# Kernel tuning notes

Hardware: AMD Instinct MI355X
Metric: run time of the kernel (lower is better)

The kernel has to match this reference:

```python
import jax, jax.numpy as jnp
import numpy as np

V, E, H, D, DFF, NB, C, B, T = 32000, 512, 256, 512, 2048, 4, 16, 32, 512
PAD, BOS, EOS = 0, 1, 2


def positional_encoding(t, d):
    pos = jnp.arange(t, dtype=jnp.float32)[:, None]
    i = jnp.arange(0, d, 2, dtype=jnp.float32)
    div = jnp.exp(-(jnp.log(10000.0)) * i / d)
    pe = jnp.zeros((t, d), jnp.float32)
    pe = pe.at[:, 0::2].set(jnp.sin(pos * div))
    pe = pe.at[:, 1::2].set(jnp.cos(pos * div))
    return pe


def layernorm(x, g, b, eps=1e-5):
    mu = jnp.mean(x, -1, keepdims=True)
    var = jnp.mean((x - mu) ** 2, -1, keepdims=True)
    return (x - mu) * jax.lax.rsqrt(var + eps) * g + b


def gru_dir(xs, w_ih, w_hh, b_ih, b_hh, reverse):
    # xs: (B,T,E); precompute input projections for all t (one big GEMM)
    gi = jnp.einsum('bte,ge->btg', xs, w_ih) + b_ih  # (B,T,3H)
    h0 = jnp.zeros((xs.shape[0], H), xs.dtype)

    def step(h, gi_t):
        gh = h @ w_hh.T + b_hh
        i_r, i_z, i_n = jnp.split(gi_t, 3, -1)
        h_r, h_z, h_n = jnp.split(gh, 3, -1)
        r = jax.nn.sigmoid(i_r + h_r)
        z = jax.nn.sigmoid(i_z + h_z)
        n = jnp.tanh(i_n + r * h_n)
        h_new = (1.0 - z) * n + z * h
        return h_new, h_new

    _, hs = jax.lax.scan(step, h0, jnp.swapaxes(gi, 0, 1), reverse=reverse)
    return jnp.swapaxes(hs, 0, 1)  # (B,T,H)


def forward(x, y, embed_W, w_ih_f, w_hh_f, b_ih_f, b_hh_f, w_ih_b, w_hh_b, b_ih_b, b_hh_b,
            ff_w1, ff_b1, ff_w2, ff_b2, ln_g, ln_b, fc_w, fc_b, trans):
    h = embed_W[x]                                   # (B,T,E)
    h = h + positional_encoding(h.shape[1], E)[None]
    hf = gru_dir(h, w_ih_f, w_hh_f, b_ih_f, b_hh_f, False)
    hb = gru_dir(h, w_ih_b, w_hh_b, b_ih_b, b_hh_b, True)
    h = jnp.concatenate([hf, hb], -1)                # (B,T,D)
    for i in range(NB):                              # FeedForward blocks (residual + LN)
        ff = jax.nn.relu(h @ ff_w1[i] + ff_b1[i]) @ ff_w2[i] + ff_b2[i]
        h = layernorm(h + ff, ln_g[i], ln_b[i])
    logits = h @ fc_w + fc_b                         # (B,T,C) emissions

    # --- CRF viterbi decode ---
    mask = (y != PAD)                                # (B,T) bool
    emit = jnp.swapaxes(logits, 0, 1)                # (T,B,C)
    m = jnp.swapaxes(mask, 0, 1)                     # (T,B)
    score0 = trans[BOS][None] + emit[0]              # (B,C)

    def vstep(score, inp):
        e_t, m_t = inp                               # (B,C), (B,)
        cand = score[:, :, None] + trans[None] + e_t[:, None, :]  # (B,prev,cur)
        new = jnp.max(cand, axis=1)
        bp = jnp.argmax(cand, axis=1)                # (B,C)
        new = jnp.where(m_t[:, None], new, score)
        return new, bp

    final, bps = jax.lax.scan(vstep, score0, (emit[1:], m[1:]))  # bps: (T-1,B,C)
    final = final + trans[:, EOS][None]
    best_score = jnp.max(final, -1)                  # (B,)
    last_tag = jnp.argmax(final, -1)                 # (B,)

    def back(tag, inp):
        bp_t, m_t = inp
        prev = jnp.take_along_axis(bp_t, tag[:, None], axis=1)[:, 0]
        prev = jnp.where(m_t, prev, tag)
        return prev, tag

    first_tag, rest = jax.lax.scan(back, last_tag, (bps, m[1:]), reverse=True)
    path = jnp.swapaxes(jnp.concatenate([first_tag[None], rest], 0), 0, 1)  # (B,T)
    return best_score, path


def setup_inputs():
    key = jax.random.key(0)
    ks = jax.random.split(key, 16)
    nrm = lambda k, sh, sc: jax.random.normal(k, sh, jnp.float32) * sc
    s = 1.0 / float(np.sqrt(H))
    inp = {}
    inp['x'] = jax.random.randint(ks[0], (B, T), 1, V)
    inp['y'] = jax.random.randint(ks[1], (B, T), 0, 13) + 3  # in [3,16): no pad/bos/eos
    inp['embed_W'] = nrm(ks[2], (V, E), 0.02)
    inp['w_ih_f'] = nrm(ks[3], (3 * H, E), s); inp['w_hh_f'] = nrm(ks[4], (3 * H, H), s)
    inp['b_ih_f'] = nrm(ks[5], (3 * H,), s); inp['b_hh_f'] = nrm(ks[6], (3 * H,), s)
    inp['w_ih_b'] = nrm(ks[7], (3 * H, E), s); inp['w_hh_b'] = nrm(ks[8], (3 * H, H), s)
    inp['b_ih_b'] = nrm(ks[9], (3 * H,), s); inp['b_hh_b'] = nrm(ks[10], (3 * H,), s)
    inp['ff_w1'] = nrm(ks[11], (NB, D, DFF), 1.0 / float(np.sqrt(D)))
    inp['ff_b1'] = jnp.zeros((NB, DFF), jnp.float32)
    inp['ff_w2'] = nrm(ks[12], (NB, DFF, D), 1.0 / float(np.sqrt(DFF)))
    inp['ff_b2'] = jnp.zeros((NB, D), jnp.float32)
    inp['ln_g'] = jnp.ones((NB, D), jnp.float32); inp['ln_b'] = jnp.zeros((NB, D), jnp.float32)
    inp['fc_w'] = nrm(ks[13], (D, C), 1.0 / float(np.sqrt(D)))
    inp['fc_b'] = jnp.zeros((C,), jnp.float32)
    inp['trans'] = nrm(ks[14], (C, C), 0.1)
    return inp


def reference(x, y, embed_W, w_ih_f, w_hh_f, b_ih_f, b_hh_f, w_ih_b, w_hh_b, b_ih_b, b_hh_b,
              ff_w1, ff_b1, ff_w2, ff_b2, ln_g, ln_b, fc_w, fc_b, trans):
    return forward(x, y, embed_W, w_ih_f, w_hh_f, b_ih_f, b_hh_f, w_ih_b, w_hh_b, b_ih_b, b_hh_b,
                   ff_w1, ff_b1, ff_w2, ff_b2, ln_g, ln_b, fc_w, fc_b, trans)
```

## Files before the change

### kernel.cpp

```cpp
#include <hip/hip_runtime.h>

#define DEV __device__ __forceinline__

using short8 = __attribute__((ext_vector_type(8))) short;
using f32x4  = __attribute__((ext_vector_type(4))) float;
using i32x4  = __attribute__((ext_vector_type(4))) int;

DEV float b2f(short s) {
  union { unsigned u; float f; } c;
  c.u = ((unsigned)(unsigned short)s) << 16;
  return c.f;
}
DEV short f2b(float f) {
  union { float f; unsigned u; } c; c.f = f;
  unsigned u = c.u + 0x7fffu + ((c.u >> 16) & 1u);
  return (short)(u >> 16);
}
DEV float fast_sigmoid(float x) {
  return __builtin_amdgcn_rcpf(1.f + __expf(-x));
}
DEV float fast_tanh(float x) {
  return 1.f - 2.f * __builtin_amdgcn_rcpf(1.f + __expf(2.f * x));
}
DEV void async_ld16(const void* g, void* lds) {
  __builtin_amdgcn_global_load_lds(
      (const __attribute__((address_space(1))) void*)(unsigned long long)g,
      (__attribute__((address_space(3))) void*)(unsigned)(unsigned long long)lds,
      16, 0, 0);
}

__global__ __launch_bounds__(256) void k_cvt2(const float* __restrict__ a, const float* __restrict__ b,
                                              short* __restrict__ oa, short* __restrict__ ob) {
  int blk = blockIdx.x;
  const float* in; short* out; int base;
  if (blk < 384) { in = a; out = oa; base = blk; }
  else           { in = b; out = ob; base = blk - 384; }
  int i = base * 256 + threadIdx.x;
  f32x4 v = *(const f32x4*)(in + (size_t)i * 4);
  short4 o;
#pragma unroll
  for (int j = 0; j < 4; j++) ((short*)&o)[j] = f2b(v[j]);
  *(short4*)(out + (size_t)i * 4) = o;
}

__global__ __launch_bounds__(256) void k_wq8(const float* __restrict__ wf,
                                             const float* __restrict__ wb,
                                             int* __restrict__ out) {
  int flat = blockIdx.x * 256 + threadIdx.x;
  int lane = flat & 63;
  int c = (flat >> 6) & 3;
  int t = flat >> 8;
  int g = t % 3;
  int t2 = t / 3;
  int v = t2 & 15, d = t2 >> 4;
  const float* w = d ? wb : wf;
  int row = g * 256 + v * 16 + (lane & 15);
  int k0 = c * 64 + (lane >> 4) * 16;
  const float* p = w + (size_t)row * 256 + k0;
  int pk[4];
#pragma unroll
  for (int i = 0; i < 4; i++) {
    f32x4 f = *(const f32x4*)(p + i * 4);
    int b0 = (int)__builtin_rintf(f[0] * 256.f);
    int b1 = (int)__builtin_rintf(f[1] * 256.f);
    int b2 = (int)__builtin_rintf(f[2] * 256.f);
    int b3 = (int)__builtin_rintf(f[3] * 256.f);
    b0 = min(127, max(-127, b0)); b1 = min(127, max(-127, b1));
    b2 = min(127, max(-127, b2)); b3 = min(127, max(-127, b3));
    pk[i] = (b0 & 255) | ((b1 & 255) << 8) | ((b2 & 255) << 16) | ((b3 & 255) << 24);
  }
  *(int4*)(out + (size_t)flat * 4) = *(int4*)pk;
}

__global__ __launch_bounds__(256) void k_embed(const int* __restrict__ x,
                                               const float* __restrict__ W,
                                               short* __restrict__ h0) {
  int flat = blockIdx.x * 256 + threadIdx.x;
  int row  = flat >> 6;
  int e0   = (flat & 63) << 3;
  int tok  = x[row];
  int t    = row & 511;
  const float* wp = W + (size_t)tok * 512 + e0;
  float v[8];
  *(f32x4*)v       = *(const f32x4*)(wp);
  *(f32x4*)(v + 4) = *(const f32x4*)(wp + 4);
  short8 o;
#pragma unroll
  for (int i = 0; i < 8; i += 2) {
    float f = expf(-9.210340371976184f * (float)(e0 + i) * (1.f / 512.f));
    float ang = (float)t * f;
    o[i]     = f2b(v[i]     + sinf(ang));
    o[i + 1] = f2b(v[i + 1] + cosf(ang));
  }
  *(short8*)(h0 + (size_t)flat * 8) = o;
}

template <int MODE>
__global__ __launch_bounds__(256) void k_gemm(const short* __restrict__ A,
    const short* __restrict__ B, const float* __restrict__ bias,
    const float* __restrict__ bias2,
    float* __restrict__ Cf, short* __restrict__ Cb, int M, int N, int K) {
  __shared__ short smA[8192];
  __shared__ short smB[8192];
  const int tid = threadIdx.x, lane = tid & 63, wave = tid >> 6;
  const int m15 = lane & 15, q8 = (lane >> 4) << 3;
  const int tn = N >> 7;
  const int bm = blockIdx.x / tn, bn = blockIdx.x % tn;
  const int wm = wave & 1, wn = wave >> 1;
  const f32x4 z4 = {0.f, 0.f, 0.f, 0.f};
  f32x4 acc[4][4];
#pragma unroll
  for (int i = 0; i < 4; i++)
#pragma unroll
    for (int j = 0; j < 4; j++) acc[i][j] = z4;

  for (int k0 = 0; k0 < K; k0 += 64) {
#pragma unroll
    for (int is = 0; is < 4; is++) {
      int c = is * 4 + wave;
      int mb = c & 7, kb = c >> 3;
      async_ld16(A + (size_t)(bm * 128 + mb * 16 + m15) * K + k0 + kb * 32 + q8, smA + c * 512);
      async_ld16(B + (size_t)(bn * 128 + mb * 16 + m15) * K + k0 + kb * 32 + q8, smB + c * 512);
    }
    __syncthreads();
#pragma unroll
    for (int kk = 0; kk < 2; kk++) {
      short8 af[4], bf[4];
#pragma unroll
      for (int i = 0; i < 4; i++)
        af[i] = *(const short8*)(smA + (kk * 8 + wm * 4 + i) * 512 + lane * 8);
#pragma unroll
      for (int j = 0; j < 4; j++)
        bf[j] = *(const short8*)(smB + (kk * 8 + wn * 4 + j) * 512 + lane * 8);
#pragma unroll
      for (int i = 0; i < 4; i++)
#pragma unroll
        for (int j = 0; j < 4; j++)
          acc[i][j] = __builtin_amdgcn_mfma_f32_16x16x32_bf16(af[i], bf[j], acc[i][j], 0, 0, 0);
    }
    __syncthreads();
  }
#pragma unroll
  for (int j = 0; j < 4; j++) {
    int col = bn * 128 + wn * 64 + j * 16 + m15;
    float bv;
    if (MODE == 3) bv = (col < 768) ? bias[col] : bias2[col - 768];
    else           bv = bias[col];
#pragma unroll
    for (int i = 0; i < 4; i++) {
      int row0 = bm * 128 + wm * 64 + i * 16 + ((lane >> 4) << 2);
#pragma unroll
      for (int r = 0; r < 4; r++) {
        float v = acc[i][j][r] + bv;
        int rr = row0 + r;
        if (MODE == 0) {
          Cf[(size_t)rr * N + col] = v;
        } else if (MODE == 1) {
          if (v < 0.f) v = 0.f;
          Cb[(size_t)rr * N + col] = f2b(v);
        } else {
          Cb[((size_t)((rr & 511) * 32 + (rr >> 9))) * 1536 + col] = f2b(v);
        }
      }
    }
  }
}

__global__ __launch_bounds__(1024) void k_gru(
    const int* __restrict__ wq8,
    const float* __restrict__ bhh_f, const float* __restrict__ bhh_b,
    const short* __restrict__ gi16,
    short* __restrict__ hcat16,
    const float* __restrict__ ff_w1, const float* __restrict__ ff_w2,
    short* __restrict__ w1t, short* __restrict__ w2t) {
  __shared__ __align__(16) char smem[16896];
  const int blk = blockIdx.x;
  const int tid = threadIdx.x;

  if (blk >= 16) {
    int sub = tid >> 8, stid = tid & 255;
    int tileid = (blk - 16) * 4 + sub;
    const float* in; short* out; int C, R, tm;
    if (tileid < 4096) { int mat = tileid >> 10; in = ff_w1 + (size_t)mat * 1048576;
                         out = w1t + (size_t)mat * 1048576; R = 512; C = 2048; tm = tileid & 1023; }
    else               { int mat = (tileid - 4096) >> 10; in = ff_w2 + (size_t)mat * 1048576;
                         out = w2t + (size_t)mat * 1048576; R = 2048; C = 512; tm = tileid & 1023; }
    float (*tile)[33] = (float(*)[33])(smem + sub * 4224);
    int ct = C >> 5;
    int bc = tm % ct, br = tm / ct;
    int r0 = br << 5, c0 = bc << 5;
    for (int i = stid; i < 1024; i += 256) {
      int r = i >> 5, c = i & 31;
      tile[r][c] = in[(size_t)(r0 + r) * C + c0 + c];
    }
    __syncthreads();
    for (int i = stid; i < 1024; i += 256) {
      int c = i >> 5, r = i & 31;
      out[(size_t)(c0 + c) * R + r0 + r] = f2b(tile[r][c]);
    }
    return;
  }

  char (*hb)[4096] = (char(*)[4096])smem;
  const int d = blk & 1, bg = blk >> 1;
  const int lane = tid & 63, v = tid >> 6;
  const int m15 = lane & 15, quad = lane >> 4;
  const int col = v * 16 + m15;
  const int brow = quad;
  const float* bhh = d ? bhh_b : bhh_f;
  const float SCL = 1.f / (127.f * 256.f);

  i32x4 Bq[3][4];
  {
    const i32x4* wp = (const i32x4*)wq8 + (size_t)(d * 16 + v) * (3 * 4 * 64);
#pragma unroll
    for (int g = 0; g < 3; g++)
#pragma unroll
      for (int c = 0; c < 4; c++)
        Bq[g][c] = wp[(g * 4 + c) * 64 + lane];
  }
  float bh[3];
#pragma unroll
  for (int g = 0; g < 3; g++) bh[g] = bhh[g * 256 + col];

  const int sw = (m15 & 7) << 4;
  const int aof0 = m15 * 256 + ((quad * 16 +   0) ^ sw);
  const int aof1 = m15 * 256 + ((quad * 16 +  64) ^ sw);
  const int aof2 = m15 * 256 + ((quad * 16 + 128) ^ sw);
  const int aof3 = m15 * 256 + ((quad * 16 + 192) ^ sw);
  const int wofs = brow * 256 + (col ^ (brow << 4));
  const int idx4 = m15 << 2;

  for (int i = tid; i < 2048; i += 1024) ((int*)hb)[i] = 0;

  const int t0 = d ? 511 : 0;
  const long gdelta = (long)(d ? -1 : 1) * 32 * 1536;
  const long hdelta = (long)(d ? -1 : 1) * 32 * 512;
  const short* gp = gi16 + ((size_t)t0 * 32 + bg * 4 + brow) * 1536 + d * 768 + col;
  short* hflush = hcat16 + ((size_t)t0 * 32 + bg * 4 + brow) * 512 + d * 256 + col;

  float gic0 = b2f(gp[0]), gic1 = b2f(gp[256]), gic2 = b2f(gp[512]);
  gp += gdelta;
  float hprev = 0.f;
  unsigned obuf[4] = {0u, 0u, 0u, 0u};
  const i32x4 zi = {0, 0, 0, 0};
  __syncthreads();

  for (int s = 0; s < 512; s++) {
    if ((s & 7) == 0 && s) {
      short* p = hflush;
#pragma unroll
      for (int k = 0; k < 8; k++) {
        *p = (short)(obuf[k >> 1] >> ((k & 1) * 16));
        p += hdelta;
      }
      hflush += 8 * hdelta;
    }
    short n0 = 0, n1 = 0, n2 = 0;
    if (s < 511) {
      n0 = gp[0]; n1 = gp[256]; n2 = gp[512];
      gp += gdelta;
    }
    const char* hs = hb[s & 1];
    i32x4 Af0 = *(const i32x4*)(hs + aof0);
    i32x4 Af1 = *(const i32x4*)(hs + aof1);
    i32x4 Af2 = *(const i32x4*)(hs + aof2);
    i32x4 Af3 = *(const i32x4*)(hs + aof3);
    i32x4 acc0 = zi, acc1 = zi, acc2 = zi;
    acc0 = __builtin_amdgcn_mfma_i32_16x16x64_i8(Af0, Bq[0][0], acc0, 0, 0, 0);
    acc1 = __builtin_amdgcn_mfma_i32_16x16x64_i8(Af0, Bq[1][0], acc1, 0, 0, 0);
    acc2 = __builtin_amdgcn_mfma_i32_16x16x64_i8(Af0, Bq[2][0], acc2, 0, 0, 0);
    acc0 = __builtin_amdgcn_mfma_i32_16x16x64_i8(Af1, Bq[0][1], acc0, 0, 0, 0);
    acc1 = __builtin_amdgcn_mfma_i32_16x16x64_i8(Af1, Bq[1][1], acc1, 0, 0, 0);
    acc2 = __builtin_amdgcn_mfma_i32_16x16x64_i8(Af1, Bq[2][1], acc2, 0, 0, 0);
    acc0 = __builtin_amdgcn_mfma_i32_16x16x64_i8(Af2, Bq[0][2], acc0, 0, 0, 0);
    acc1 = __builtin_amdgcn_mfma_i32_16x16x64_i8(Af2, Bq[1][2], acc1, 0, 0, 0);
    acc2 = __builtin_amdgcn_mfma_i32_16x16x64_i8(Af2, Bq[2][2], acc2, 0, 0, 0);
    acc0 = __builtin_amdgcn_mfma_i32_16x16x64_i8(Af3, Bq[0][3], acc0, 0, 0, 0);
    acc1 = __builtin_amdgcn_mfma_i32_16x16x64_i8(Af3, Bq[1][3], acc1, 0, 0, 0);
    acc2 = __builtin_amdgcn_mfma_i32_16x16x64_i8(Af3, Bq[2][3], acc2, 0, 0, 0);
    int r0 = __builtin_amdgcn_ds_bpermute(idx4, acc0[0]);
    int r1 = __builtin_amdgcn_ds_bpermute(idx4, acc0[1]);
    int r2 = __builtin_amdgcn_ds_bpermute(idx4, acc0[2]);
    int r3 = __builtin_amdgcn_ds_bpermute(idx4, acc0[3]);
    int z0 = __builtin_amdgcn_ds_bpermute(idx4, acc1[0]);
    int z1 = __builtin_amdgcn_ds_bpermute(idx4, acc1[1]);
    int z2 = __builtin_amdgcn_ds_bpermute(idx4, acc1[2]);
    int z3 = __builtin_amdgcn_ds_bpermute(idx4, acc1[3]);
    int n0i = __builtin_amdgcn_ds_bpermute(idx4, acc2[0]);
    int n1i = __builtin_amdgcn_ds_bpermute(idx4, acc2[1]);
    int n2i = __builtin_amdgcn_ds_bpermute(idx4, acc2[2]);
    int n3i = __builtin_amdgcn_ds_bpermute(idx4, acc2[3]);
    int igr = (quad & 2) ? ((quad & 1) ? r3 : r2) : ((quad & 1) ? r1 : r0);
    int igz = (quad & 2) ? ((quad & 1) ? z3 : z2) : ((quad & 1) ? z1 : z0);
    int ign = (quad & 2) ? ((quad & 1) ? n3i : n2i) : ((quad & 1) ? n1i : n0i);
    float r = fast_sigmoid(fmaf((float)igr, SCL, gic0 + bh[0]));
    float z = fast_sigmoid(fmaf((float)igz, SCL, gic1 + bh[1]));
    float n = fast_tanh(fmaf(r, fmaf((float)ign, SCL, bh[2]), gic2));
    float h = (1.f - z) * n + z * hprev;
    hprev = h;
    int hq = (int)__builtin_rintf(h * 127.f);
    hb[(s + 1) & 1][wofs] = (char)hq;
    unsigned hb16 = (unsigned)(unsigned short)f2b(h);
    int idx = s & 7;
    if ((idx & 1) == 0) obuf[idx >> 1] = hb16;
    else                obuf[idx >> 1] |= hb16 << 16;
    gic0 = b2f(n0); gic1 = b2f(n1); gic2 = b2f(n2);
    __syncthreads();
  }
  {
    short* p = hflush;
#pragma unroll
    for (int k = 0; k < 8; k++) {
      *p = (short)(obuf[k >> 1] >> ((k & 1) * 16));
      p += hdelta;
    }
  }
}

template <int FIRST>
__global__ __launch_bounds__(256) void k_ln(const float* __restrict__ hinf,
    const float* __restrict__ ff, const float* __restrict__ gw,
    const float* __restrict__ bw, float* __restrict__ hout, short* __restrict__ h16) {
  int row = blockIdx.x * 4 + (threadIdx.x >> 6);
  int lane = threadIdx.x & 63;
  size_t base = (size_t)row * 512 + lane * 8;
  f32x4 x0, x1;
  if (FIRST) {
    short8 hv = *(const short8*)(h16 + base);
#pragma unroll
    for (int i = 0; i < 4; i++) { x0[i] = b2f(hv[i]); x1[i] = b2f(hv[4 + i]); }
  } else {
    x0 = *(const f32x4*)(hinf + base);
    x1 = *(const f32x4*)(hinf + base + 4);
  }
  f32x4 y0 = *(const f32x4*)(ff + base);
  f32x4 y1 = *(const f32x4*)(ff + base + 4);
  x0 += y0; x1 += y1;
  float s = x0[0] + x0[1] + x0[2] + x0[3] + x1[0] + x1[1] + x1[2] + x1[3];
#pragma unroll
  for (int off = 32; off >= 1; off >>= 1) s += __shfl_xor(s, off);
  float mu = s * (1.f / 512.f);
  float vv = 0.f;
#pragma unroll
  for (int i = 0; i < 4; i++) { float d0 = x0[i] - mu, d1 = x1[i] - mu; vv += d0 * d0 + d1 * d1; }
#pragma unroll
  for (int off = 32; off >= 1; off >>= 1) vv += __shfl_xor(vv, off);
  float rs = rsqrtf(vv * (1.f / 512.f) + 1e-5f);
  int e = lane * 8;
  f32x4 g0 = *(const f32x4*)(gw + e), g1 = *(const f32x4*)(gw + e + 4);
  f32x4 bb0 = *(const f32x4*)(bw + e), bb1 = *(const f32x4*)(bw + e + 4);
  f32x4 o0, o1; short8 ob;
#pragma unroll
  for (int i = 0; i < 4; i++) {
    float a = (x0[i] - mu) * rs * g0[i] + bb0[i];
    float b = (x1[i] - mu) * rs * g1[i] + bb1[i];
    o0[i] = a; o1[i] = b; ob[i] = f2b(a); ob[4 + i] = f2b(b);
  }
  *(f32x4*)(hout + base) = o0;
  *(f32x4*)(hout + base + 4) = o1;
  *(short8*)(h16 + base) = ob;
}

__global__ __launch_bounds__(256) void k_fc(const float* __restrict__ h,
    const float* __restrict__ fcw, const float* __restrict__ bias,
    float* __restrict__ logits) {
  int row = blockIdx.x * 4 + (threadIdx.x >> 6);
  int lane = threadIdx.x & 63;
  int c = lane & 15, part = lane >> 4;
  const float* ph = h + (size_t)row * 512 + part * 128;
  const float* pw = fcw + (size_t)part * 128 * 16 + c;
  float acc = 0.f;
#pragma unroll 8
  for (int k = 0; k < 128; k += 4) {
    f32x4 hv = *(const f32x4*)(ph + k);
    acc += hv[0] * pw[(k) * 16] + hv[1] * pw[(k + 1) * 16]
         + hv[2] * pw[(k + 2) * 16] + hv[3] * pw[(k + 3) * 16];
  }
  acc += __shfl_xor(acc, 16);
  acc += __shfl_xor(acc, 32);
  if (part == 0) logits[(size_t)row * 16 + c] = acc + bias[c];
}

__global__ __launch_bounds__(64) void k_crf(const float* __restrict__ logits,
    const int* __restrict__ y, const float* __restrict__ trans,
    float* __restrict__ out) {
  __shared__ unsigned char bp[511][16];
  int b = blockIdx.x, lane = threadIdx.x;
  int cur = lane & 15, g = lane >> 4;
  float trr0 = trans[(4 * g + 0) * 16 + cur];
  float trr1 = trans[(4 * g + 1) * 16 + cur];
  float trr2 = trans[(4 * g + 2) * 16 + cur];
  float trr3 = trans[(4 * g + 3) * 16 + cur];
  const float* lg = logits + (size_t)b * 16;
  const int* yb = y + b * 512;
  float score = trans[16 + cur] + lg[cur];
  float e_next = lg[512 + cur];
  int y_next = yb[1];
  for (int t = 1; t < 512; t++) {
    float e = e_next; int ym = y_next;
    if (t < 511) { e_next = lg[(t + 1) * 512 + cur]; y_next = yb[t + 1]; }
    float s0 = __shfl(score, 4 * g + 0);
    float s1 = __shfl(score, 4 * g + 1);
    float s2 = __shfl(score, 4 * g + 2);
    float s3 = __shfl(score, 4 * g + 3);
    float best = s0 + trr0; int arg = 4 * g;
    float c1 = s1 + trr1; if (c1 > best) { best = c1; arg = 4 * g + 1; }
    float c2 = s2 + trr2; if (c2 > best) { best = c2; arg = 4 * g + 2; }
    float c3 = s3 + trr3; if (c3 > best) { best = c3; arg = 4 * g + 3; }
    float pv = __shfl_xor(best, 16); int pa = __shfl_xor(arg, 16);
    bool take = (lane & 16) ? (pv >= best) : (pv > best);
    if (take) { best = pv; arg = pa; }
    pv = __shfl_xor(best, 32); pa = __shfl_xor(arg, 32);
    take = (lane & 32) ? (pv >= best) : (pv > best);
    if (take) { best = pv; arg = pa; }
    if (lane < 16) bp[t - 1][cur] = (unsigned char)arg;
    float ns = best + e;
    if (ym == 0) ns = score;
    score = ns;
  }
  score += trans[cur * 16 + 2];
  float best = -3.4e38f; int argb = 0;
#pragma unroll
  for (int p = 0; p < 16; p++) {
    float sp = __shfl(score, p);
    if (sp > best) { best = sp; argb = p; }
  }
  __syncthreads();
  if (lane == 0) {
    out[b] = best;
    float* po = out + 32 + (size_t)b * 512;
    int tag = argb;
    po[511] = (float)tag;
    for (int t = 511; t >= 1; t--) {
      int prev = bp[t - 1][tag];
      if (yb[t] == 0) prev = tag;
      po[t - 1] = (float)prev;
      tag = prev;
    }
  }
}

extern "C" void kernel_launch(void* const* d_in, const int* in_sizes, int n_in,
                              void* d_out, int out_size, void* d_ws, size_t ws_size,
                              hipStream_t stream) {
  const int*   x      = (const int*)d_in[0];
  const int*   y      = (const int*)d_in[1];
  const float* embedW = (const float*)d_in[2];
  const float* w_ih_f = (const float*)d_in[3];
  const float* w_hh_f = (const float*)d_in[4];
  const float* b_ih_f = (const float*)d_in[5];
  const float* b_hh_f = (const float*)d_in[6];
  const float* w_ih_b = (const float*)d_in[7];
  const float* w_hh_b = (const float*)d_in[8];
  const float* b_ih_b = (const float*)d_in[9];
  const float* b_hh_b = (const float*)d_in[10];
  const float* ff_w1  = (const float*)d_in[11];
  const float* ff_b1  = (const float*)d_in[12];
  const float* ff_w2  = (const float*)d_in[13];
  const float* ff_b2  = (const float*)d_in[14];
  const float* ln_g   = (const float*)d_in[15];
  const float* ln_b   = (const float*)d_in[16];
  const float* fc_w   = (const float*)d_in[17];
  const float* fc_b   = (const float*)d_in[18];
  const float* trans  = (const float*)d_in[19];
  float* out = (float*)d_out;

  char* ws = (char*)d_ws;
  short* h0     = (short*)(ws + 0);
  short* gi16   = (short*)(ws + 16777216);
  short* mid    = (short*)(ws + 16777216);
  float* ffout  = (float*)(ws + 83886080);
  short* wihf16 = (short*)(ws + 117440512);
  short* wihb16 = (short*)(ws + 118226944);
  int*   wq8    = (int*)  (ws + 119013376);
  short* w1t    = (short*)(ws + 119799808);
  short* w2t    = (short*)(ws + 128188416);
  short* hcat16 = (short*)(ws + 136577024);
  float* hres   = (float*)(ws + 153354240);
  float* logits = (float*)(ws + 186908672);

  k_embed<<<4096, 256, 0, stream>>>(x, embedW, h0);
  k_cvt2<<<768, 256, 0, stream>>>(w_ih_f, w_ih_b, wihf16, wihb16);
  k_wq8<<<96, 256, 0, stream>>>(w_hh_f, w_hh_b, wq8);

  k_gemm<3><<<1536, 256, 0, stream>>>(h0, wihf16, b_ih_f, b_ih_b, nullptr, gi16, 16384, 1536, 512);

  k_gru<<<2064, 1024, 0, stream>>>(wq8, b_hh_f, b_hh_b, gi16, hcat16,
                                   ff_w1, ff_w2, w1t, w2t);

  for (int i = 0; i < 4; i++) {
    k_gemm<1><<<2048, 256, 0, stream>>>(hcat16, w1t + (size_t)i * 1048576, ff_b1 + i * 2048,
                                        nullptr, nullptr, mid, 16384, 2048, 512);
    k_gemm<0><<<512, 256, 0, stream>>>(mid, w2t + (size_t)i * 1048576, ff_b2 + i * 512,
                                       nullptr, ffout, nullptr, 16384, 512, 2048);
    if (i == 0)
      k_ln<1><<<4096, 256, 0, stream>>>(nullptr, ffout, ln_g, ln_b, hres, hcat16);
    else
      k_ln<0><<<4096, 256, 0, stream>>>(hres, ffout, ln_g + i * 512, ln_b + i * 512, hres, hcat16);
  }
  k_fc<<<4096, 256, 0, stream>>>(hres, fc_w, fc_b, logits);
  k_crf<<<32, 64, 0, stream>>>(logits, y, trans, out);
}
```

Before: 1.520 ms.

## Move FF weight transpose into input GEMM, vectorize epilogue, bf16 FF output

The FF weight transpose/convert work moves out of the GRU launch and into extra blocks of the input-projection GEMM, so the GRU kernel launches only its 16 recurrent blocks. The GEMM gains an XCD-aware block index remap, swaps MFMA operands so each lane owns four contiguous columns, and stores with vectorized short4/f32x4 writes. The second FF GEMM now writes bf16 instead of fp32, halving the traffic into layernorm at the cost of reduced precision in the residual add. The transpose no longer overlaps the serial GRU, which risks adding time on the critical path.

New measurement: 1.602 ms. 5.4% more time.

```diff
diff --git a/kernel.cpp b/kernel.cpp
--- a/kernel.cpp
+++ b/kernel.cpp
@@ -99,13 +99,43 @@
 __global__ __launch_bounds__(256) void k_gemm(const short* __restrict__ A,
     const short* __restrict__ B, const float* __restrict__ bias,
     const float* __restrict__ bias2,
-    float* __restrict__ Cf, short* __restrict__ Cb, int M, int N, int K) {
-  __shared__ short smA[8192];
-  __shared__ short smB[8192];
+    float* __restrict__ Cf, short* __restrict__ Cb, int M, int N, int K,
+    const float* __restrict__ tw1, const float* __restrict__ tw2,
+    short* __restrict__ w1t, short* __restrict__ w2t) {
+  __shared__ __align__(16) char smem[32768];
+  short* smA = (short*)smem;
+  short* smB = (short*)smem + 8192;
+  const int blk0 = blockIdx.x;
+
+  if (MODE == 3 && blk0 >= 1536) {
+    int tileid = blk0 - 1536;
+    const float* in; short* out; int R, C, tm;
+    if (tileid < 4096) { int mat = tileid >> 10; in = tw1 + (size_t)mat * 1048576;
+                         out = w1t + (size_t)mat * 1048576; R = 512; C = 2048; tm = tileid & 1023; }
+    else               { int mat = (tileid - 4096) >> 10; in = tw2 + (size_t)mat * 1048576;
+                         out = w2t + (size_t)mat * 1048576; R = 2048; C = 512; tm = tileid & 1023; }
+    float (*tile)[33] = (float(*)[33])smem;
+    int ct = C >> 5;
+    int bc = tm % ct, br = tm / ct;
+    int r0 = br << 5, c0 = bc << 5;
+    for (int i = threadIdx.x; i < 1024; i += 256) {
+      int r = i >> 5, c = i & 31;
+      tile[r][c] = in[(size_t)(r0 + r) * C + c0 + c];
+    }
+    __syncthreads();
+    for (int i = threadIdx.x; i < 1024; i += 256) {
+      int c = i >> 5, r = i & 31;
+      out[(size_t)(c0 + c) * R + r0 + r] = f2b(tile[r][c]);
+    }
+    return;
+  }
+
+  const int ngemm = (MODE == 3) ? 1536 : gridDim.x;
+  const int blk = (blk0 % 8) * (ngemm >> 3) + (blk0 >> 3);
   const int tid = threadIdx.x, lane = tid & 63, wave = tid >> 6;
-  const int m15 = lane & 15, q8 = (lane >> 4) << 3;
+  const int m15 = lane & 15, quad = lane >> 4, q8 = quad << 3;
   const int tn = N >> 7;
-  const int bm = blockIdx.x / tn, bn = blockIdx.x % tn;
+  const int bm = blk / tn, bn = blk % tn;
   const int wm = wave & 1, wn = wave >> 1;
   const f32x4 z4 = {0.f, 0.f, 0.f, 0.f};
   f32x4 acc[4][4];
@@ -136,31 +166,42 @@
       for (int i = 0; i < 4; i++)
 #pragma unroll
         for (int j = 0; j < 4; j++)
-          acc[i][j] = __builtin_amdgcn_mfma_f32_16x16x32_bf16(af[i], bf[j], acc[i][j], 0, 0, 0);
+          acc[i][j] = __builtin_amdgcn_mfma_f32_16x16x32_bf16(bf[j], af[i], acc[i][j], 0, 0, 0);
     }
     __syncthreads();
   }
 #pragma unroll
   for (int j = 0; j < 4; j++) {
-    int col = bn * 128 + wn * 64 + j * 16 + m15;
-    float bv;
-    if (MODE == 3) bv = (col < 768) ? bias[col] : bias2[col - 768];
-    else           bv = bias[col];
+    int col0 = bn * 128 + wn * 64 + j * 16 + quad * 4;
+    f32x4 bv4;
+    if (MODE == 3) {
+      const float* bp = (col0 < 768) ? (bias + col0) : (bias2 + (col0 - 768));
+      bv4 = *(const f32x4*)bp;
+    } else {
+      bv4 = *(const f32x4*)(bias + col0);
+    }
 #pragma unroll
     for (int i = 0; i < 4; i++) {
-      int row0 = bm * 128 + wm * 64 + i * 16 + ((lane >> 4) << 2);
-#pragma unroll
-      for (int r = 0; r < 4; r++) {
-        float v = acc[i][j][r] + bv;
-        int rr = row0 + r;
-        if (MODE == 0) {
-          Cf[(size_t)rr * N + col] = v;
-        } else if (MODE == 1) {
-          if (v < 0.f) v = 0.f;
-          Cb[(size_t)rr * N + col] = f2b(v);
-        } else {
-          Cb[((size_t)((rr & 511) * 32 + (rr >> 9))) * 1536 + col] = f2b(v);
+      int row = bm * 128 + wm * 64 + i * 16 + m15;
+      f32x4 v;
+#pragma unroll
+      for (int r = 0; r < 4; r++) v[r] = acc[i][j][r] + bv4[r];
+      if (MODE == 1 || MODE == 4) {
+        short4 o;
+#pragma unroll
+        for (int r = 0; r < 4; r++) {
+          float x = v[r];
+          if (MODE == 1 && x < 0.f) x = 0.f;
+          ((short*)&o)[r] = f2b(x);
         }
+        *(short4*)(Cb + (size_t)row * N + col0) = o;
+      } else if (MODE == 3) {
+        short4 o;
+#pragma unroll
+        for (int r = 0; r < 4; r++) ((short*)&o)[r] = f2b(v[r]);
+        *(short4*)(Cb + ((size_t)((row & 511) * 32 + (row >> 9))) * 1536 + col0) = o;
+      } else {
+        *(f32x4*)(Cf + (size_t)row * N + col0) = v;
       }
     }
   }
@@ -170,40 +211,11 @@
     const int* __restrict__ wq8,
     const float* __restrict__ bhh_f, const float* __restrict__ bhh_b,
     const short* __restrict__ gi16,
-    short* __restrict__ hcat16,
-    const float* __restrict__ ff_w1, const float* __restrict__ ff_w2,
-    short* __restrict__ w1t, short* __restrict__ w2t) {
-  __shared__ __align__(16) char smem[16896];
+    short* __restrict__ hcat16) {
+  __shared__ __align__(16) char hb[2][4096];
   const int blk = blockIdx.x;
-  const int tid = threadIdx.x;
-
-  if (blk >= 16) {
-    int sub = tid >> 8, stid = tid & 255;
-    int tileid = (blk - 16) * 4 + sub;
-    const float* in; short* out; int C, R, tm;
-    if (tileid < 4096) { int mat = tileid >> 10; in = ff_w1 + (size_t)mat * 1048576;
-                         out = w1t + (size_t)mat * 1048576; R = 512; C = 2048; tm = tileid & 1023; }
-    else               { int mat = (tileid - 4096) >> 10; in = ff_w2 + (size_t)mat * 1048576;
-                         out = w2t + (size_t)mat * 1048576; R = 2048; C = 512; tm = tileid & 1023; }
-    float (*tile)[33] = (float(*)[33])(smem + sub * 4224);
-    int ct = C >> 5;
-    int bc = tm % ct, br = tm / ct;
-    int r0 = br << 5, c0 = bc << 5;
-    for (int i = stid; i < 1024; i += 256) {
-      int r = i >> 5, c = i & 31;
-      tile[r][c] = in[(size_t)(r0 + r) * C + c0 + c];
-    }
-    __syncthreads();
-    for (int i = stid; i < 1024; i += 256) {
-      int c = i >> 5, r = i & 31;
-      out[(size_t)(c0 + c) * R + r0 + r] = f2b(tile[r][c]);
-    }
-    return;
-  }
-
-  char (*hb)[4096] = (char(*)[4096])smem;
   const int d = blk & 1, bg = blk >> 1;
-  const int lane = tid & 63, v = tid >> 6;
+  const int tid = threadIdx.x, lane = tid & 63, v = tid >> 6;
   const int m15 = lane & 15, quad = lane >> 4;
   const int col = v * 16 + m15;
   const int brow = quad;
@@ -320,7 +332,7 @@
 
 template <int FIRST>
 __global__ __launch_bounds__(256) void k_ln(const float* __restrict__ hinf,
-    const float* __restrict__ ff, const float* __restrict__ gw,
+    const short* __restrict__ ff16, const float* __restrict__ gw,
     const float* __restrict__ bw, float* __restrict__ hout, short* __restrict__ h16) {
   int row = blockIdx.x * 4 + (threadIdx.x >> 6);
   int lane = threadIdx.x & 63;
@@ -334,9 +346,9 @@
     x0 = *(const f32x4*)(hinf + base);
     x1 = *(const f32x4*)(hinf + base + 4);
   }
-  f32x4 y0 = *(const f32x4*)(ff + base);
-  f32x4 y1 = *(const f32x4*)(ff + base + 4);
-  x0 += y0; x1 += y1;
+  short8 fv = *(const short8*)(ff16 + base);
+#pragma unroll
+  for (int i = 0; i < 4; i++) { x0[i] += b2f(fv[i]); x1[i] += b2f(fv[4 + i]); }
   float s = x0[0] + x0[1] + x0[2] + x0[3] + x1[0] + x1[1] + x1[2] + x1[3];
 #pragma unroll
   for (int off = 32; off >= 1; off >>= 1) s += __shfl_xor(s, off);
@@ -470,7 +482,7 @@
   short* h0     = (short*)(ws + 0);
   short* gi16   = (short*)(ws + 16777216);
   short* mid    = (short*)(ws + 16777216);
-  float* ffout  = (float*)(ws + 83886080);
+  short* ffout16= (short*)(ws + 83886080);
   short* wihf16 = (short*)(ws + 117440512);
   short* wihb16 = (short*)(ws + 118226944);
   int*   wq8    = (int*)  (ws + 119013376);
@@ -484,20 +496,22 @@
   k_cvt2<<<768, 256, 0, stream>>>(w_ih_f, w_ih_b, wihf16, wihb16);
   k_wq8<<<96, 256, 0, stream>>>(w_hh_f, w_hh_b, wq8);
 
-  k_gemm<3><<<1536, 256, 0, stream>>>(h0, wihf16, b_ih_f, b_ih_b, nullptr, gi16, 16384, 1536, 512);
-
-  k_gru<<<2064, 1024, 0, stream>>>(wq8, b_hh_f, b_hh_b, gi16, hcat16,
-                                   ff_w1, ff_w2, w1t, w2t);
+  k_gemm<3><<<9728, 256, 0, stream>>>(h0, wihf16, b_ih_f, b_ih_b, nullptr, gi16,
+                                      16384, 1536, 512, ff_w1, ff_w2, w1t, w2t);
+
+  k_gru<<<16, 1024, 0, stream>>>(wq8, b_hh_f, b_hh_b, gi16, hcat16);
 
   for (int i = 0; i < 4; i++) {
     k_gemm<1><<<2048, 256, 0, stream>>>(hcat16, w1t + (size_t)i * 1048576, ff_b1 + i * 2048,
-                                        nullptr, nullptr, mid, 16384, 2048, 512);
-    k_gemm<0><<<512, 256, 0, stream>>>(mid, w2t + (size_t)i * 1048576, ff_b2 + i * 512,
-                                       nullptr, ffout, nullptr, 16384, 512, 2048);
+                                        nullptr, nullptr, mid, 16384, 2048, 512,
+                                        nullptr, nullptr, nullptr, nullptr);
+    k_gemm<4><<<512, 256, 0, stream>>>(mid, w2t + (size_t)i * 1048576, ff_b2 + i * 512,
+                                       nullptr, nullptr, ffout16, 16384, 512, 2048,
+                                       nullptr, nullptr, nullptr, nullptr);
     if (i == 0)
-      k_ln<1><<<4096, 256, 0, stream>>>(nullptr, ffout, ln_g, ln_b, hres, hcat16);
+      k_ln<1><<<4096, 256, 0, stream>>>(nullptr, ffout16, ln_g, ln_b, hres, hcat16);
     else
-      k_ln<0><<<4096, 256, 0, stream>>>(hres, ffout, ln_g + i * 512, ln_b + i * 512, hres, hcat16);
+      k_ln<0><<<4096, 256, 0, stream>>>(hres, ffout16, ln_g + i * 512, ln_b + i * 512, hres, hcat16);
   }
   k_fc<<<4096, 256, 0, stream>>>(hres, fc_w, fc_b, logits);
   k_crf<<<32, 64, 0, stream>>>(logits, y, trans, out);
```
